# Performance work log

Hardware: AMD Instinct MI355X
Metric: run time of the kernel (lower is better)

The kernel has to match this reference:

```python
import jax, jax.numpy as jnp
import numpy as np

N_NODES = 10000
N_EDGES = 640000
NF = 128      # n_features
NH = 128      # n_hidden
NT = 128      # n_targets
LN_EPS = 1e-5


def _layer_norm(h, gamma, beta):
    mu = jnp.mean(h, axis=-1, keepdims=True)
    var = jnp.var(h, axis=-1, keepdims=True)
    return (h - mu) * jax.lax.rsqrt(var + LN_EPS) * gamma + beta


def _mlp(h, W1, b1, gamma, beta, W2, b2):
    h = jax.nn.relu(h @ W1 + b1)
    h = _layer_norm(h, gamma, beta)
    return h @ W2 + b2


def setup_inputs() -> dict:
    key = jax.random.key(0)
    ks = jax.random.split(key, 12)
    s_in = 1.0 / np.sqrt(NF + NH)
    s_h = 1.0 / np.sqrt(NH)
    return {
        "x": jax.random.normal(ks[0], (N_NODES, NF), dtype=jnp.float32),
        "edge_idx": jax.random.randint(ks[1], (2, N_EDGES), 0, N_NODES, dtype=jnp.int32),
        "edge_attr": jax.random.normal(ks[2], (N_EDGES, NH), dtype=jnp.float32),
        # node_mlp_1 params
        "W1a": jax.random.normal(ks[3], (NF + NH, NH), dtype=jnp.float32) * s_in,
        "b1a": jnp.zeros((NH,), dtype=jnp.float32),
        "g1": jnp.ones((NH,), dtype=jnp.float32),
        "be1": jnp.zeros((NH,), dtype=jnp.float32),
        "W1b": jax.random.normal(ks[4], (NH, NH), dtype=jnp.float32) * s_h,
        "b1b": jnp.zeros((NH,), dtype=jnp.float32),
        # node_mlp_2 params
        "W2a": jax.random.normal(ks[5], (NF + NH, NH), dtype=jnp.float32) * s_in,
        "b2a": jnp.zeros((NH,), dtype=jnp.float32),
        "g2": jnp.ones((NH,), dtype=jnp.float32),
        "be2": jnp.zeros((NH,), dtype=jnp.float32),
        "W2b": jax.random.normal(ks[6], (NH, NT), dtype=jnp.float32) * s_h,
        "b2b": jnp.zeros((NT,), dtype=jnp.float32),
    }


def reference(x, edge_idx, edge_attr, W1a, b1a, g1, be1, W1b, b1b,
              W2a, b2a, g2, be2, W2b, b2b):
    row, col = edge_idx[0], edge_idx[1]
    # gather source-node features and run per-edge MLP
    h = jnp.concatenate([x[col], edge_attr], axis=1)        # [E, NF+NH]
    h = _mlp(h, W1a, b1a, g1, be1, W1b, b1b)                 # [E, NH]
    # scatter_mean into target nodes
    sums = jax.ops.segment_sum(h, row, num_segments=N_NODES)
    cnt = jax.ops.segment_sum(jnp.ones((h.shape[0],), h.dtype), row,
                              num_segments=N_NODES)
    agg = sums / jnp.maximum(cnt, 1.0)[:, None]              # [N, NH]
    out = jnp.concatenate([x, agg], axis=1)                  # [N, NF+NH]
    return _mlp(out, W2a, b2a, g2, be2, W2b, b2b)            # [N, NT]
```

## Files before the change

kernel.cpp:

```cpp
#include <hip/hip_runtime.h>
#include <hip/hip_bf16.h>

#define NN 10000
#define NE 640000
#define NF 128
#define NH 128
#define NT 128
#define KA 256
#define LN_EPS 1e-5f

typedef __bf16 bf16x8 __attribute__((ext_vector_type(8)));
typedef float floatx4 __attribute__((ext_vector_type(4)));
typedef float nfloat4 __attribute__((ext_vector_type(4)));

__device__ inline unsigned short f2bf(float f) {
    unsigned int u = __float_as_uint(f);
    u += 0x7FFFu + ((u >> 16) & 1u);
    return (unsigned short)(u >> 16);
}

__device__ inline bf16x8 load_frag(const unsigned short* p) {
    uint4 u = *(const uint4*)p;
    return __builtin_bit_cast(bf16x8, u);
}

__device__ inline floatx4 mfma16(bf16x8 a, bf16x8 b, floatx4 c) {
    return __builtin_amdgcn_mfma_f32_16x16x32_bf16(a, b, c, 0, 0, 0);
}

__device__ inline bf16x8 cvt8(nfloat4 v0, nfloat4 v1) {
    bf16x8 r;
    r[0] = (__bf16)v0.x; r[1] = (__bf16)v0.y; r[2] = (__bf16)v0.z; r[3] = (__bf16)v0.w;
    r[4] = (__bf16)v1.x; r[5] = (__bf16)v1.y; r[6] = (__bf16)v1.z; r[7] = (__bf16)v1.w;
    return r;
}

__device__ inline void lds_fence() {
    asm volatile("s_waitcnt lgkmcnt(0)" ::: "memory");
    __builtin_amdgcn_sched_barrier(0);
}

__global__ __launch_bounds__(256) void prep_kernel(
    const float* __restrict__ x,
    const int* __restrict__ erow,
    const float* __restrict__ W1a, const float* __restrict__ W1b,
    const float* __restrict__ W2a, const float* __restrict__ W2b,
    unsigned short* __restrict__ wp1a, unsigned short* __restrict__ wp1b,
    unsigned short* __restrict__ wp2a, unsigned short* __restrict__ wp2b,
    unsigned short* __restrict__ xbf, int* __restrict__ hist)
{
    const int tid = blockIdx.x * 256 + threadIdx.x;
    const int nth = gridDim.x * 256;

    for (int e = tid; e < NE; e += nth)
        atomicAdd(&hist[erow[e]], 1);

    const nfloat4* xs = (const nfloat4*)x;
    uint4* xd = (uint4*)xbf;
    for (int i = tid; i < 160000; i += nth)
        xd[i] = __builtin_bit_cast(uint4, cvt8(xs[2 * i], xs[2 * i + 1]));

    if (tid < 12288) {
        const float* src; unsigned short* dst; int t, nks;
        if (tid < 4096)       { src = W1a; dst = wp1a; t = tid;         nks = 8; }
        else if (tid < 6144)  { src = W1b; dst = wp1b; t = tid - 4096;  nks = 4; }
        else if (tid < 10240) { src = W2a; dst = wp2a; t = tid - 6144;  nks = 8; }
        else                  { src = W2b; dst = wp2b; t = tid - 10240; nks = 4; }
        const int f = t >> 6, l = t & 63;
        const int ct = f / nks, ks = f - ct * nks;
        const int n  = ct * 16 + (l & 15);
        const int k0 = ks * 32 + (l >> 4) * 8;
        unsigned short tmp[8];
#pragma unroll
        for (int j = 0; j < 8; ++j)
            tmp[j] = f2bf(src[(k0 + j) * 128 + n]);
        *(uint4*)&dst[t * 8] = *(const uint4*)tmp;
    }
}

__global__ __launch_bounds__(256) void scan_kernel(
    const int* __restrict__ hist, int* __restrict__ row_start,
    int* __restrict__ cursor)
{
    __shared__ int partials[256];
    const int t = threadIdx.x;
    const int base = t * 40;
    int s = 0;
    for (int i = 0; i < 40; ++i) {
        int b = base + i;
        if (b < NN) s += hist[b];
    }
    partials[t] = s;
    __syncthreads();
    int pre = 0;
    for (int i = 0; i < t; ++i) pre += partials[i];
    int run = pre;
    for (int i = 0; i < 40; ++i) {
        int b = base + i;
        if (b < NN) {
            row_start[b] = run;
            cursor[b] = run;
            run += hist[b];
        }
    }
    if (t == 255) row_start[NN] = NE;
}

__global__ __launch_bounds__(256) void scatter_kernel(
    const int* __restrict__ row, int* __restrict__ cursor,
    int* __restrict__ perm)
{
    int e = blockIdx.x * 256 + threadIdx.x;
    if (e < NE) {
        int p = atomicAdd(&cursor[row[e]], 1);
        perm[p] = e;
    }
}

__global__ __launch_bounds__(256, 4) void edge_mlp_kernel(
    const unsigned short* __restrict__ xbf,
    const int* __restrict__ erow, const int* __restrict__ ecol,
    const float* __restrict__ eattr,
    const int* __restrict__ perm,
    const unsigned short* __restrict__ wp1a, const float* __restrict__ b1a,
    const float* __restrict__ g1, const float* __restrict__ be1,
    float* __restrict__ H)
{
    __shared__ __align__(16) float smem[64 * 132];
    __shared__ int rows_s[64];

    const int wave = threadIdx.x >> 6;
    const int lane = threadIdx.x & 63;
    const int lm   = lane & 15;
    const int lq4  = lane >> 4;
    const int e0   = blockIdx.x * 64;

    unsigned short* At = (unsigned short*)smem;

    if (threadIdx.x < 64)
        rows_s[threadIdx.x] = erow[perm[e0 + threadIdx.x]];

    {
        const int lrow = lane >> 2;
        const int lq   = lane & 3;
        const int e = perm[e0 + wave * 16 + lrow];
        const int scol = ecol[e];
        const uint4* xr = (const uint4*)(xbf + (size_t)scol * NF);
        const nfloat4* ar = (const nfloat4*)(eattr + (size_t)e * NH);
        unsigned short* Ar = At + (wave * 16 + lrow) * 264;
#pragma unroll
        for (int it = 0; it < 4; ++it) {
            const int g = lq + it * 4;
            *(uint4*)&Ar[g * 8] = xr[g];
        }
#pragma unroll
        for (int it = 0; it < 4; ++it) {
            const int g = lq + it * 4;
            nfloat4 v0 = __builtin_nontemporal_load(ar + g * 2);
            nfloat4 v1 = __builtin_nontemporal_load(ar + g * 2 + 1);
            *(uint4*)&Ar[128 + g * 8] = __builtin_bit_cast(uint4, cvt8(v0, v1));
        }
    }
    lds_fence();

    bf16x8 a1[8];
#pragma unroll
    for (int ks = 0; ks < 8; ++ks)
        a1[ks] = load_frag(&At[(wave * 16 + lm) * 264 + ks * 32 + lq4 * 8]);

    floatx4 acc1[8];
#pragma unroll
    for (int ct = 0; ct < 8; ++ct) {
        floatx4 acc = {0.f, 0.f, 0.f, 0.f};
        const unsigned short* wr = wp1a + (ct * 8 * 64 + lane) * 8;
#pragma unroll
        for (int ks = 0; ks < 8; ++ks) {
            bf16x8 b = load_frag(wr + ks * 512);
            acc = mfma16(a1[ks], b, acc);
        }
        acc1[ct] = acc;
    }

    float sum_[4] = {0, 0, 0, 0}, sq_[4] = {0, 0, 0, 0};
#pragma unroll
    for (int ct = 0; ct < 8; ++ct) {
        const float bb = b1a[ct * 16 + lm];
#pragma unroll
        for (int i = 0; i < 4; ++i) {
            float v = acc1[ct][i] + bb;
            v = fmaxf(v, 0.f);
            acc1[ct][i] = v;
            sum_[i] += v;
            sq_[i]  += v * v;
        }
    }
#pragma unroll
    for (int m = 1; m < 16; m <<= 1) {
#pragma unroll
        for (int i = 0; i < 4; ++i) {
            sum_[i] += __shfl_xor(sum_[i], m, 64);
            sq_[i]  += __shfl_xor(sq_[i],  m, 64);
        }
    }
    float mu[4], rs[4];
#pragma unroll
    for (int i = 0; i < 4; ++i) {
        mu[i] = sum_[i] * (1.f / NH);
        float var = sq_[i] * (1.f / NH) - mu[i] * mu[i];
        rs[i] = rsqrtf(var + LN_EPS);
    }

#pragma unroll
    for (int ct = 0; ct < 8; ++ct) {
        const int c = ct * 16 + lm;
        const float gg = g1[c], bb = be1[c];
#pragma unroll
        for (int i = 0; i < 4; ++i) {
            const int r = wave * 16 + lq4 * 4 + i;
            smem[r * 132 + c] = (acc1[ct][i] - mu[i]) * rs[i] * gg + bb;
        }
    }
    __syncthreads();

    {
        const int t = threadIdx.x;
        const int cc = t & 127;
        const int jb = (t >> 7) * 32;
        float a = 0.f;
        int cur = rows_s[jb];
#pragma unroll 4
        for (int j = jb; j < jb + 32; ++j) {
            a += smem[j * 132 + cc];
            int nxt = (j + 1 < jb + 32) ? rows_s[j + 1] : -1;
            if (nxt != cur) {
                atomicAdd(&H[cur * NH + cc], a);
                a = 0.f;
                cur = nxt;
            }
        }
    }
}

__global__ __launch_bounds__(64) void node_mlp_kernel(
    const unsigned short* __restrict__ xbf,
    const float* __restrict__ H, const int* __restrict__ row_start,
    const float* __restrict__ b1b, const unsigned short* __restrict__ wp1b,
    const unsigned short* __restrict__ wp2a, const float* __restrict__ b2a,
    const float* __restrict__ g2, const float* __restrict__ be2,
    const unsigned short* __restrict__ wp2b, const float* __restrict__ b2b,
    float* __restrict__ out)
{
    __shared__ unsigned short Atile[16][KA + 8];
    __shared__ unsigned short Ttile[16][NH + 8];
    __shared__ float addb_s[16];

    const int lane = threadIdx.x;
    const int lm   = lane & 15;
    const int lq4  = lane >> 4;
    const int n0   = blockIdx.x * 16;

    {
        const int lrow = lane >> 2;
        const int lq   = lane & 3;
        int n = n0 + lrow;
        if (n >= NN) n = NN - 1;
        const int cntn = row_start[n + 1] - row_start[n];
        const float inv  = (cntn > 0) ? (1.f / (float)cntn) : 1.f;
        if (lq == 0) addb_s[lrow] = (cntn > 0) ? 1.f : 0.f;
        const uint4* xr = (const uint4*)(xbf + (size_t)n * NF);
        const nfloat4* hr = (const nfloat4*)(H + (size_t)n * NH);
#pragma unroll
        for (int it = 0; it < 4; ++it) {
            const int g = lq + it * 4;
            *(uint4*)&Atile[lrow][g * 8] = xr[g];
            nfloat4 v0 = hr[g * 2], v1 = hr[g * 2 + 1];
            nfloat4 u0, u1;
            u0.x = v0.x * inv; u0.y = v0.y * inv; u0.z = v0.z * inv; u0.w = v0.w * inv;
            u1.x = v1.x * inv; u1.y = v1.y * inv; u1.z = v1.z * inv; u1.w = v1.w * inv;
            *(uint4*)&Ttile[lrow][g * 8] = __builtin_bit_cast(uint4, cvt8(u0, u1));
        }
    }
    lds_fence();

    {
        bf16x8 ah[4];
#pragma unroll
        for (int ks = 0; ks < 4; ++ks)
            ah[ks] = load_frag(&Ttile[lm][ks * 32 + lq4 * 8]);
#pragma unroll
        for (int ct = 0; ct < 8; ++ct) {
            floatx4 acc = {0.f, 0.f, 0.f, 0.f};
            const unsigned short* wr = wp1b + (ct * 4 * 64 + lane) * 8;
#pragma unroll
            for (int ks = 0; ks < 4; ++ks) {
                bf16x8 b = load_frag(wr + ks * 512);
                acc = mfma16(ah[ks], b, acc);
            }
            const int c = ct * 16 + lm;
            const float bb = b1b[c];
#pragma unroll
            for (int i = 0; i < 4; ++i) {
                float av = acc[i] + addb_s[lq4 * 4 + i] * bb;
                Atile[lq4 * 4 + i][128 + c] = f2bf(av);
            }
        }
    }
    lds_fence();

    bf16x8 a1[8];
#pragma unroll
    for (int ks = 0; ks < 8; ++ks)
        a1[ks] = load_frag(&Atile[lm][ks * 32 + lq4 * 8]);

    floatx4 acc1[8];
#pragma unroll
    for (int ct = 0; ct < 8; ++ct) {
        floatx4 acc = {0.f, 0.f, 0.f, 0.f};
        const unsigned short* wr = wp2a + (ct * 8 * 64 + lane) * 8;
#pragma unroll
        for (int ks = 0; ks < 8; ++ks) {
            bf16x8 b = load_frag(wr + ks * 512);
            acc = mfma16(a1[ks], b, acc);
        }
        acc1[ct] = acc;
    }

    float sum_[4] = {0, 0, 0, 0}, sq_[4] = {0, 0, 0, 0};
#pragma unroll
    for (int ct = 0; ct < 8; ++ct) {
        const float bb = b2a[ct * 16 + lm];
#pragma unroll
        for (int i = 0; i < 4; ++i) {
            float v = acc1[ct][i] + bb;
            v = fmaxf(v, 0.f);
            acc1[ct][i] = v;
            sum_[i] += v;
            sq_[i]  += v * v;
        }
    }
#pragma unroll
    for (int m = 1; m < 16; m <<= 1) {
#pragma unroll
        for (int i = 0; i < 4; ++i) {
            sum_[i] += __shfl_xor(sum_[i], m, 64);
            sq_[i]  += __shfl_xor(sq_[i],  m, 64);
        }
    }
    float mu[4], rs[4];
#pragma unroll
    for (int i = 0; i < 4; ++i) {
        mu[i] = sum_[i] * (1.f / NH);
        float var = sq_[i] * (1.f / NH) - mu[i] * mu[i];
        rs[i] = rsqrtf(var + LN_EPS);
    }
#pragma unroll
    for (int ct = 0; ct < 8; ++ct) {
        const int c = ct * 16 + lm;
        const float gg = g2[c], bb = be2[c];
#pragma unroll
        for (int i = 0; i < 4; ++i) {
            float nv = (acc1[ct][i] - mu[i]) * rs[i] * gg + bb;
            Ttile[lq4 * 4 + i][c] = f2bf(nv);
        }
    }
    lds_fence();

    bf16x8 a2[4];
#pragma unroll
    for (int ks = 0; ks < 4; ++ks)
        a2[ks] = load_frag(&Ttile[lm][ks * 32 + lq4 * 8]);

#pragma unroll
    for (int ct = 0; ct < 8; ++ct) {
        floatx4 acc = {0.f, 0.f, 0.f, 0.f};
        const unsigned short* wr = wp2b + (ct * 4 * 64 + lane) * 8;
#pragma unroll
        for (int ks = 0; ks < 4; ++ks) {
            bf16x8 b = load_frag(wr + ks * 512);
            acc = mfma16(a2[ks], b, acc);
        }
        const int c = ct * 16 + lm;
        const float bb = b2b[c];
#pragma unroll
        for (int i = 0; i < 4; ++i) {
            int n = n0 + lq4 * 4 + i;
            if (n < NN) out[n * NT + c] = acc[i] + bb;
        }
    }
}

extern "C" void kernel_launch(void* const* d_in, const int* in_sizes, int n_in,
                              void* d_out, int out_size, void* d_ws, size_t ws_size,
                              hipStream_t stream) {
    const float* x     = (const float*)d_in[0];
    const int*   eidx  = (const int*)d_in[1];
    const float* eattr = (const float*)d_in[2];
    const float* W1a = (const float*)d_in[3];
    const float* b1a = (const float*)d_in[4];
    const float* g1  = (const float*)d_in[5];
    const float* be1 = (const float*)d_in[6];
    const float* W1b = (const float*)d_in[7];
    const float* b1b = (const float*)d_in[8];
    const float* W2a = (const float*)d_in[9];
    const float* b2a = (const float*)d_in[10];
    const float* g2  = (const float*)d_in[11];
    const float* be2 = (const float*)d_in[12];
    const float* W2b = (const float*)d_in[13];
    const float* b2b = (const float*)d_in[14];

    char* ws = (char*)d_ws;
    float* H         = (float*)ws;
    int*   hist      = (int*)(ws + 5120000);
    int*   cursor    = (int*)(ws + 5160000);
    int*   row_start = (int*)(ws + 5200000);
    int*   perm      = (int*)(ws + 5240064);
    unsigned short* wp1a = (unsigned short*)(ws + 7800064);
    unsigned short* wp1b = (unsigned short*)(ws + 7865600);
    unsigned short* wp2a = (unsigned short*)(ws + 7898368);
    unsigned short* wp2b = (unsigned short*)(ws + 7963904);
    unsigned short* xbf  = (unsigned short*)(ws + 7996672);

    const int* erow = eidx;
    const int* ecol = eidx + NE;

    (void)hipMemsetAsync(ws, 0, 5160000, stream);
    prep_kernel<<<640, 256, 0, stream>>>(x, erow, W1a, W1b, W2a, W2b,
                                         wp1a, wp1b, wp2a, wp2b, xbf, hist);
    scan_kernel<<<1, 256, 0, stream>>>(hist, row_start, cursor);
    scatter_kernel<<<(NE + 255) / 256, 256, 0, stream>>>(erow, cursor, perm);
    edge_mlp_kernel<<<NE / 64, 256, 0, stream>>>(xbf, erow, ecol, eattr, perm,
                                                 wp1a, b1a, g1, be1, H);
    node_mlp_kernel<<<(NN + 15) / 16, 64, 0, stream>>>(xbf, H, row_start,
                                                       b1b, wp1b,
                                                       wp2a, b2a, g2, be2,
                                                       wp2b, b2b,
                                                       (float*)d_out);
}
```

Before: 687.4 us.

## Precompute per-node x@W1a projection and gather it per edge

Splits the first edge-MLP matmul: the x[col] half of W1a is applied once per node (10k nodes) inside the scatter kernel, with the bias folded in, and stored as fp32 xw. The edge kernel then gathers the projected 128-float row per edge as the initial accumulator and runs only the edge_attr half of the K dimension through MFMA. This halves per-edge MFMA work and LDS staging, but the per-edge gather now reads fp32 rows instead of bf16, doubling gather bytes. Numerics shift slightly because the x contribution is no longer rounded through bf16 A-tiles in the same way.

After: 663.8 us. 1.04x faster.

```diff
diff --git a/kernel.cpp b/kernel.cpp
--- a/kernel.cpp
+++ b/kernel.cpp
@@ -108,21 +108,65 @@
 
 __global__ __launch_bounds__(256) void scatter_kernel(
     const int* __restrict__ row, int* __restrict__ cursor,
-    int* __restrict__ perm)
+    int* __restrict__ perm,
+    const unsigned short* __restrict__ xbf,
+    const unsigned short* __restrict__ wp1a, const float* __restrict__ b1a,
+    float* __restrict__ xw)
 {
+    __shared__ unsigned short Xt[16][136];
+
     int e = blockIdx.x * 256 + threadIdx.x;
     if (e < NE) {
         int p = atomicAdd(&cursor[row[e]], 1);
         perm[p] = e;
     }
+
+    if (blockIdx.x < 625 && threadIdx.x < 64) {
+        const int lane = threadIdx.x;
+        const int lm   = lane & 15;
+        const int lq4  = lane >> 4;
+        const int n0   = blockIdx.x * 16;
+        {
+            const int lrow = lane >> 2;
+            const int lq   = lane & 3;
+            const uint4* xr = (const uint4*)(xbf + (size_t)(n0 + lrow) * NF);
+#pragma unroll
+            for (int it = 0; it < 4; ++it) {
+                const int g = lq + it * 4;
+                *(uint4*)&Xt[lrow][g * 8] = xr[g];
+            }
+        }
+        lds_fence();
+
+        bf16x8 a[4];
+#pragma unroll
+        for (int ks = 0; ks < 4; ++ks)
+            a[ks] = load_frag(&Xt[lm][ks * 32 + lq4 * 8]);
+
+#pragma unroll
+        for (int ct = 0; ct < 8; ++ct) {
+            floatx4 acc = {0.f, 0.f, 0.f, 0.f};
+            const unsigned short* wr = wp1a + ((ct * 8) * 64 + lane) * 8;
+#pragma unroll
+            for (int ks = 0; ks < 4; ++ks) {
+                bf16x8 b = load_frag(wr + ks * 512);
+                acc = mfma16(a[ks], b, acc);
+            }
+            const int c = ct * 16 + lm;
+            const float bb = b1a[c];
+#pragma unroll
+            for (int i = 0; i < 4; ++i)
+                xw[(size_t)(n0 + lq4 * 4 + i) * NH + c] = acc[i] + bb;
+        }
+    }
 }
 
 __global__ __launch_bounds__(256, 4) void edge_mlp_kernel(
-    const unsigned short* __restrict__ xbf,
+    const float* __restrict__ xw,
     const int* __restrict__ erow, const int* __restrict__ ecol,
     const float* __restrict__ eattr,
     const int* __restrict__ perm,
-    const unsigned short* __restrict__ wp1a, const float* __restrict__ b1a,
+    const unsigned short* __restrict__ wp1a,
     const float* __restrict__ g1, const float* __restrict__ be1,
     float* __restrict__ H)
 {
@@ -144,37 +188,42 @@
         const int lrow = lane >> 2;
         const int lq   = lane & 3;
         const int e = perm[e0 + wave * 16 + lrow];
-        const int scol = ecol[e];
-        const uint4* xr = (const uint4*)(xbf + (size_t)scol * NF);
         const nfloat4* ar = (const nfloat4*)(eattr + (size_t)e * NH);
-        unsigned short* Ar = At + (wave * 16 + lrow) * 264;
-#pragma unroll
-        for (int it = 0; it < 4; ++it) {
-            const int g = lq + it * 4;
-            *(uint4*)&Ar[g * 8] = xr[g];
-        }
+        unsigned short* Ar = At + (wave * 16 + lrow) * 136;
 #pragma unroll
         for (int it = 0; it < 4; ++it) {
             const int g = lq + it * 4;
             nfloat4 v0 = __builtin_nontemporal_load(ar + g * 2);
             nfloat4 v1 = __builtin_nontemporal_load(ar + g * 2 + 1);
-            *(uint4*)&Ar[128 + g * 8] = __builtin_bit_cast(uint4, cvt8(v0, v1));
-        }
-    }
+            *(uint4*)&Ar[g * 8] = __builtin_bit_cast(uint4, cvt8(v0, v1));
+        }
+    }
+
+    int scol_own = 0;
+    if (lane < 16) scol_own = ecol[perm[e0 + wave * 16 + lane]];
+    floatx4 acc1[8];
+#pragma unroll
+    for (int i = 0; i < 4; ++i) {
+        const int sc = __shfl(scol_own, lq4 * 4 + i, 64);
+        const float* xr = xw + (size_t)sc * NH + lm;
+#pragma unroll
+        for (int ct = 0; ct < 8; ++ct)
+            acc1[ct][i] = xr[ct * 16];
+    }
+
     lds_fence();
 
-    bf16x8 a1[8];
-#pragma unroll
-    for (int ks = 0; ks < 8; ++ks)
-        a1[ks] = load_frag(&At[(wave * 16 + lm) * 264 + ks * 32 + lq4 * 8]);
-
-    floatx4 acc1[8];
-#pragma unroll
-    for (int ct = 0; ct < 8; ++ct) {
-        floatx4 acc = {0.f, 0.f, 0.f, 0.f};
-        const unsigned short* wr = wp1a + (ct * 8 * 64 + lane) * 8;
-#pragma unroll
-        for (int ks = 0; ks < 8; ++ks) {
+    bf16x8 a1[4];
+#pragma unroll
+    for (int ks = 0; ks < 4; ++ks)
+        a1[ks] = load_frag(&At[(wave * 16 + lm) * 136 + ks * 32 + lq4 * 8]);
+
+#pragma unroll
+    for (int ct = 0; ct < 8; ++ct) {
+        floatx4 acc = acc1[ct];
+        const unsigned short* wr = wp1a + ((ct * 8 + 4) * 64 + lane) * 8;
+#pragma unroll
+        for (int ks = 0; ks < 4; ++ks) {
             bf16x8 b = load_frag(wr + ks * 512);
             acc = mfma16(a1[ks], b, acc);
         }
@@ -184,11 +233,9 @@
     float sum_[4] = {0, 0, 0, 0}, sq_[4] = {0, 0, 0, 0};
 #pragma unroll
     for (int ct = 0; ct < 8; ++ct) {
-        const float bb = b1a[ct * 16 + lm];
-#pragma unroll
-        for (int i = 0; i < 4; ++i) {
-            float v = acc1[ct][i] + bb;
-            v = fmaxf(v, 0.f);
+#pragma unroll
+        for (int i = 0; i < 4; ++i) {
+            float v = fmaxf(acc1[ct][i], 0.f);
             acc1[ct][i] = v;
             sum_[i] += v;
             sq_[i]  += v * v;
@@ -419,6 +466,7 @@
     unsigned short* wp2a = (unsigned short*)(ws + 7898368);
     unsigned short* wp2b = (unsigned short*)(ws + 7963904);
     unsigned short* xbf  = (unsigned short*)(ws + 7996672);
+    float* xw        = (float*)(ws + 10556672);
 
     const int* erow = eidx;
     const int* ecol = eidx + NE;
@@ -427,9 +475,10 @@
     prep_kernel<<<640, 256, 0, stream>>>(x, erow, W1a, W1b, W2a, W2b,
                                          wp1a, wp1b, wp2a, wp2b, xbf, hist);
     scan_kernel<<<1, 256, 0, stream>>>(hist, row_start, cursor);
-    scatter_kernel<<<(NE + 255) / 256, 256, 0, stream>>>(erow, cursor, perm);
-    edge_mlp_kernel<<<NE / 64, 256, 0, stream>>>(xbf, erow, ecol, eattr, perm,
-                                                 wp1a, b1a, g1, be1, H);
+    scatter_kernel<<<(NE + 255) / 256, 256, 0, stream>>>(erow, cursor, perm,
+                                                         xbf, wp1a, b1a, xw);
+    edge_mlp_kernel<<<NE / 64, 256, 0, stream>>>(xw, erow, ecol, eattr, perm,
+                                                 wp1a, g1, be1, H);
     node_mlp_kernel<<<(NN + 15) / 16, 64, 0, stream>>>(xbf, H, row_start,
                                                        b1b, wp1b,
                                                        wp2a, b2a, g2, be2,
```
